# Kernel optimization log

Measured on AMD Instinct MI355X. Metric: run time of the kernel, lower is better.

The kernel has to match this reference:

```python
import jax, jax.numpy as jnp
import numpy as np

B, N, D, E, R, K = 4, 2048, 1024, 8, 256, 2


def setup_inputs() -> dict:
    key = jax.random.key(0)
    ks = jax.random.split(key, 5)
    scale = 0.02
    return {
        "x": jax.random.normal(ks[0], (B, N, D), dtype=jnp.float32),
        "gate_w": jax.random.normal(ks[1], (D, E), dtype=jnp.float32) * scale,
        "Wu": jax.random.normal(ks[2], (E, D, R), dtype=jnp.float32) * scale,
        "Wv": jax.random.normal(ks[3], (E, D, R), dtype=jnp.float32) * scale,
        "Wo": jax.random.normal(ks[4], (E, R, D), dtype=jnp.float32) * scale,
    }


def reference(x, gate_w, Wu, Wv, Wo):
    # Router: top-k over expert logits, softmax over the selected k logits.
    logits = jnp.einsum("bnd,de->bne", x, gate_w)          # [B,N,E]
    topv, topi = jax.lax.top_k(logits, K)                    # [B,N,K]
    w = jax.nn.softmax(topv, axis=-1)                        # [B,N,K]

    # Dense all-expert SwiGLU (matches reference semantics: every expert
    # computed for every token, then gathered by top-k index).
    u = jnp.einsum("bnd,edr->bner", x, Wu)                  # [B,N,E,R]
    v = jnp.einsum("bnd,edr->bner", x, Wv)                  # [B,N,E,R]
    s = jax.nn.silu(u) * v                                   # [B,N,E,R]
    Y = jnp.einsum("bner,erd->bned", s, Wo)                 # [B,N,E,D]

    # Gather the k selected experts per token and combine with gate weights.
    y_sel = jnp.take_along_axis(Y, topi[..., None], axis=2)  # [B,N,K,D]
    out = jnp.einsum("bnkd,bnk->bnd", y_sel, w)             # [B,N,D]
    return out
```

## Files before the change

### kernel.cpp

```cpp
#include <hip/hip_runtime.h>
#include <math.h>

#define BN 8192
#define DIM 1024
#define NE 8
#define RR 256

using bf16x8 = __attribute__((ext_vector_type(8))) short;
using f32x4  = __attribute__((ext_vector_type(4))) float;

__device__ inline unsigned short f2bf(float f) {
    unsigned int u = __float_as_uint(f);
    u = (u + 0x7fffu + ((u >> 16) & 1u)) >> 16;
    return (unsigned short)u;
}

__global__ __launch_bounds__(256) void k_gwt(const float* __restrict__ gw,
                                             float* __restrict__ gwT) {
    int i = blockIdx.x * 256 + threadIdx.x;
    float v = gw[i];
    int d = i >> 3, e = i & 7;
    gwT[e * DIM + d] = v;
}

__global__ __launch_bounds__(256) void k_router3(const float* __restrict__ x,
                                                 const float* __restrict__ gwT,
                                                 int* __restrict__ topi,
                                                 float* __restrict__ topw,
                                                 unsigned short* __restrict__ xb) {
    int wid  = (blockIdx.x * blockDim.x + threadIdx.x) >> 6;
    int lane = threadIdx.x & 63;
    const float* xp = x + (size_t)wid * DIM + lane * 4;
    unsigned short* xbp = xb + (size_t)wid * DIM + lane * 4;
    float4 acc[NE];
#pragma unroll
    for (int e = 0; e < NE; ++e) acc[e] = float4{0.f, 0.f, 0.f, 0.f};
#pragma unroll
    for (int k = 0; k < 4; ++k) {
        float4 xv = *(const float4*)(xp + k * 256);
        ushort4 us = { f2bf(xv.x), f2bf(xv.y), f2bf(xv.z), f2bf(xv.w) };
        *(ushort4*)(xbp + k * 256) = us;
#pragma unroll
        for (int e = 0; e < NE; ++e) {
            float4 gv = *(const float4*)(gwT + e * DIM + k * 256 + lane * 4);
            acc[e].x += xv.x * gv.x; acc[e].y += xv.y * gv.y;
            acc[e].z += xv.z * gv.z; acc[e].w += xv.w * gv.w;
        }
    }
    float lg[NE];
#pragma unroll
    for (int e = 0; e < NE; ++e)
        lg[e] = (acc[e].x + acc[e].y) + (acc[e].z + acc[e].w);
#pragma unroll
    for (int off = 32; off; off >>= 1) {
#pragma unroll
        for (int e = 0; e < NE; ++e) lg[e] += __shfl_xor(lg[e], off, 64);
    }
    if (lane == 0) {
        float best = lg[0]; int bi = 0;
#pragma unroll
        for (int e = 1; e < NE; ++e) if (lg[e] > best) { best = lg[e]; bi = e; }
        float sec = -3.4e38f; int si = 0;
#pragma unroll
        for (int e = 0; e < NE; ++e) if (e != bi && lg[e] > sec) { sec = lg[e]; si = e; }
        float p  = __expf(sec - best);
        float w0 = 1.f / (1.f + p);
        float w1 = p * w0;
        topi[wid * 2 + 0] = bi;  topw[wid * 2 + 0] = w0;
        topi[wid * 2 + 1] = si;  topw[wid * 2 + 1] = w1;
    }
}

__global__ __launch_bounds__(1024) void k_count_scan(const int* __restrict__ topi,
                                                     int* __restrict__ counts,
                                                     int* __restrict__ offsets,
                                                     int* __restrict__ fill,
                                                     int* __restrict__ tileOff) {
    __shared__ int sh[1024 * NE];
    int tid = threadIdx.x;
    int c[NE];
#pragma unroll
    for (int j = 0; j < NE; ++j) c[j] = 0;
    const int4* tp = (const int4*)topi;
    for (int i = tid; i < BN * 2 / 4; i += 1024) {
        int4 v = tp[i];
#pragma unroll
        for (int j = 0; j < NE; ++j)
            c[j] += (v.x == j) + (v.y == j) + (v.z == j) + (v.w == j);
    }
#pragma unroll
    for (int j = 0; j < NE; ++j) sh[tid * NE + j] = c[j];
    __syncthreads();
    for (int s = 512; s > 0; s >>= 1) {
        if (tid < s) {
#pragma unroll
            for (int j = 0; j < NE; ++j) sh[tid * NE + j] += sh[(tid + s) * NE + j];
        }
        __syncthreads();
    }
    if (tid == 0) {
        int acc = 0, tacc = 0;
        for (int j = 0; j < NE; ++j) {
            int cj = sh[j];
            counts[j]  = cj;
            offsets[j] = acc;   acc  += cj;
            tileOff[j] = tacc;  tacc += (cj + 63) >> 6;
        }
        tileOff[NE] = tacc;
    }
    if (tid < NE) fill[tid] = 0;
}

__global__ __launch_bounds__(256) void k_fill2(const int* __restrict__ topi,
                                               const float* __restrict__ topw,
                                               const int* __restrict__ offsets,
                                               int* __restrict__ fill,
                                               int* __restrict__ btok,
                                               float* __restrict__ bw,
                                               int* __restrict__ slotOf) {
    int tid = threadIdx.x;
    int i = blockIdx.x * 256 + tid;
    int w = tid >> 6, lane = tid & 63;
    int e = topi[i];
    float wt = topw[i];

    __shared__ int waveCnt[4][NE];
    __shared__ int wavePre[4][NE];
    __shared__ int baseSh[NE];

    int myrank = 0;
    unsigned long long lt = (1ull << lane) - 1ull;
#pragma unroll
    for (int j = 0; j < NE; ++j) {
        unsigned long long m = __ballot(e == j);
        if (e == j) myrank = __popcll(m & lt);
        if (lane == 0) waveCnt[w][j] = __popcll(m);
    }
    __syncthreads();
    if (tid < NE) {
        int j = tid, acc = 0;
#pragma unroll
        for (int ww = 0; ww < 4; ++ww) { wavePre[ww][j] = acc; acc += waveCnt[ww][j]; }
        baseSh[j] = atomicAdd(&fill[j], acc);
    }
    __syncthreads();
    int slot = offsets[e] + baseSh[e] + wavePre[w][e] + myrank;
    btok[slot] = i >> 1;
    bw[slot]   = wt;
    slotOf[i]  = slot;
}

__global__ __launch_bounds__(256) void k_cvt3(const float* __restrict__ Wu,
                                              const float* __restrict__ Wv,
                                              const float* __restrict__ Wo,
                                              unsigned short* __restrict__ Wub,
                                              unsigned short* __restrict__ Wvb,
                                              unsigned short* __restrict__ Wob) {
    int z = blockIdx.y;
    int which = z >> 3, e = z & 7;
    int tile = blockIdx.x;
    const float* in; unsigned short* out;
    int M, N, n0, m0;
    if (which < 2) {
        M = DIM; N = RR;
        n0 = (tile & 7) * 32;  m0 = (tile >> 3) * 32;
        in = which ? Wv : Wu;  out = which ? Wvb : Wub;
    } else {
        M = RR; N = DIM;
        n0 = (tile & 31) * 32; m0 = (tile >> 5) * 32;
        in = Wo; out = Wob;
    }
    __shared__ float t[32][33];
    int tx = threadIdx.x & 31, ty = threadIdx.x >> 5;
    const float* inE = in + (size_t)e * M * N;
    unsigned short* outE = out + (size_t)e * M * N;
#pragma unroll
    for (int i = ty; i < 32; i += 8)
        t[i][tx] = inE[(size_t)(m0 + i) * N + n0 + tx];
    __syncthreads();
#pragma unroll
    for (int i = ty; i < 32; i += 8)
        outE[(size_t)(n0 + i) * M + m0 + tx] = f2bf(t[tx][i]);
}

__global__ __launch_bounds__(256, 2) void k_uv(
        const unsigned short* __restrict__ xb,
        const unsigned short* __restrict__ Wub,
        const unsigned short* __restrict__ Wvb,
        const int* __restrict__ counts,
        const int* __restrict__ offsets,
        const int* __restrict__ tileOff,
        const int* __restrict__ btok,
        const float* __restrict__ bw,
        unsigned short* __restrict__ Sbuf) {
    int bid = blockIdx.x;
    int lt  = (bid & 7) * 66 + (bid >> 3);
    int rh  = lt & 1;
    int mt_lin = lt >> 1;
    if (mt_lin >= tileOff[NE]) return;
    int e = 0;
#pragma unroll
    for (int j = 1; j < NE; ++j) if (mt_lin >= tileOff[j]) e = j;
    int t0 = (mt_lin - tileOff[e]) * 64;
    int ne = counts[e];
    int nt = min(64, ne - t0);
    int start = offsets[e] + t0;

    int tid = threadIdx.x;
    int w = tid >> 6, lane = tid & 63;
    int m16 = lane & 15, quad = lane >> 4;

    __shared__ unsigned short As[2][64][72];
    __shared__ int   tokL[64];
    __shared__ float gwL[64];

    if (tid < 64) {
        tokL[tid] = (tid < nt) ? btok[start + tid] : btok[start];
        gwL[tid]  = (tid < nt) ? bw[start + tid] : 0.f;
    }
    __syncthreads();

    const unsigned short* WuE = Wub + (size_t)e * RR * DIM;
    const unsigned short* WvE = Wvb + (size_t)e * RR * DIM;

    int arow = tid >> 2, apart = tid & 3;
    const unsigned short* asrc = xb + (size_t)tokL[arow] * DIM + apart * 16;

    const unsigned short* buBase = WuE + (size_t)(rh * 128 + w * 32 + m16) * DIM + quad * 8;
    const unsigned short* bvBase = WvE + (size_t)(rh * 128 + w * 32 + m16) * DIM + quad * 8;

    f32x4 accU[4][2], accV[4][2];
    f32x4 zz = {0.f, 0.f, 0.f, 0.f};
#pragma unroll
    for (int mt = 0; mt < 4; ++mt)
#pragma unroll
        for (int nl = 0; nl < 2; ++nl) { accU[mt][nl] = zz; accV[mt][nl] = zz; }

    uint4 pa0 = *(const uint4*)(asrc);
    uint4 pa1 = *(const uint4*)(asrc + 8);
    uint4 bu[2][2][2], bv[2][2][2];
#pragma unroll
    for (int ks = 0; ks < 2; ++ks)
#pragma unroll
        for (int nl = 0; nl < 2; ++nl) {
            bu[0][ks][nl] = *(const uint4*)(buBase + (size_t)nl * 16 * DIM + ks * 32);
            bv[0][ks][nl] = *(const uint4*)(bvBase + (size_t)nl * 16 * DIM + ks * 32);
        }

#pragma unroll
    for (int kt = 0; kt < 16; ++kt) {
        const int cur = kt & 1, nxt = cur ^ 1;
        *(uint4*)&As[cur][arow][apart * 16]     = pa0;
        *(uint4*)&As[cur][arow][apart * 16 + 8] = pa1;
        if (kt < 15) {
            pa0 = *(const uint4*)(asrc + (kt + 1) * 64);
            pa1 = *(const uint4*)(asrc + (kt + 1) * 64 + 8);
#pragma unroll
            for (int ks = 0; ks < 2; ++ks)
#pragma unroll
                for (int nl = 0; nl < 2; ++nl) {
                    bu[nxt][ks][nl] = *(const uint4*)(buBase + (size_t)nl * 16 * DIM + (kt + 1) * 64 + ks * 32);
                    bv[nxt][ks][nl] = *(const uint4*)(bvBase + (size_t)nl * 16 * DIM + (kt + 1) * 64 + ks * 32);
                }
        }
        __syncthreads();
#pragma unroll
        for (int ks = 0; ks < 2; ++ks) {
            bf16x8 a[4];
#pragma unroll
            for (int mt = 0; mt < 4; ++mt)
                a[mt] = *(const bf16x8*)&As[cur][mt * 16 + m16][ks * 32 + quad * 8];
#pragma unroll
            for (int nl = 0; nl < 2; ++nl) {
                bf16x8 fu = __builtin_bit_cast(bf16x8, bu[cur][ks][nl]);
                bf16x8 fv = __builtin_bit_cast(bf16x8, bv[cur][ks][nl]);
#pragma unroll
                for (int mt = 0; mt < 4; ++mt) {
                    accU[mt][nl] = __builtin_amdgcn_mfma_f32_16x16x32_bf16(a[mt], fu, accU[mt][nl], 0, 0, 0);
                    accV[mt][nl] = __builtin_amdgcn_mfma_f32_16x16x32_bf16(a[mt], fv, accV[mt][nl], 0, 0, 0);
                }
            }
        }
    }

#pragma unroll
    for (int mt = 0; mt < 4; ++mt)
#pragma unroll
        for (int nl = 0; nl < 2; ++nl)
#pragma unroll
            for (int reg = 0; reg < 4; ++reg) {
                int trow = mt * 16 + quad * 4 + reg;
                int rcol = rh * 128 + w * 32 + nl * 16 + m16;
                float u = accU[mt][nl][reg], v = accV[mt][nl][reg];
                float s = (u / (1.f + __expf(-u))) * v * gwL[trow];
                if (trow < nt)
                    Sbuf[(size_t)(start + trow) * RR + rcol] = f2bf(s);
            }
}

__global__ __launch_bounds__(256, 2) void k_down(
        const unsigned short* __restrict__ Sbuf,
        const unsigned short* __restrict__ Wob,
        const int* __restrict__ counts,
        const int* __restrict__ offsets,
        const int* __restrict__ tileOff,
        const int* __restrict__ btok,
        float* __restrict__ ybuf,
        float* __restrict__ out) {
    int bid = blockIdx.x;
    int lt  = (bid & 7) * 132 + (bid >> 3);
    int nd = lt & 3;
    int mt_lin = lt >> 2;
    if (mt_lin >= tileOff[NE]) return;
    int e = 0;
#pragma unroll
    for (int j = 1; j < NE; ++j) if (mt_lin >= tileOff[j]) e = j;
    int t0 = (mt_lin - tileOff[e]) * 64;
    int ne = counts[e];
    int nt = min(64, ne - t0);
    int start = offsets[e] + t0;

    int tid = threadIdx.x;
    int w = tid >> 6, lane = tid & 63;
    int m16 = lane & 15, quad = lane >> 4;

    __shared__ unsigned short As[2][64][72];
    __shared__ int tokL[64];

    if (tid < 64)
        tokL[tid] = (tid < nt) ? btok[start + tid] : btok[start];
    __syncthreads();

    const unsigned short* WoE = Wob + (size_t)e * DIM * RR;

    int arow = tid >> 2, apart = tid & 3;
    const unsigned short* asrc = Sbuf + (size_t)(start + arow) * RR + apart * 16;

    const unsigned short* bBase = WoE + (size_t)(nd * 256 + w * 64 + m16) * RR + quad * 8;

    f32x4 acc[4][4];
    f32x4 zz = {0.f, 0.f, 0.f, 0.f};
#pragma unroll
    for (int mt = 0; mt < 4; ++mt)
#pragma unroll
        for (int nl = 0; nl < 4; ++nl) acc[mt][nl] = zz;

    uint4 pa0 = *(const uint4*)(asrc);
    uint4 pa1 = *(const uint4*)(asrc + 8);
    uint4 b[2][2][4];
#pragma unroll
    for (int ks = 0; ks < 2; ++ks)
#pragma unroll
        for (int nl = 0; nl < 4; ++nl)
            b[0][ks][nl] = *(const uint4*)(bBase + (size_t)nl * 16 * RR + ks * 32);

#pragma unroll
    for (int kt = 0; kt < 4; ++kt) {
        const int cur = kt & 1, nxt = cur ^ 1;
        *(uint4*)&As[cur][arow][apart * 16]     = pa0;
        *(uint4*)&As[cur][arow][apart * 16 + 8] = pa1;
        if (kt < 3) {
            pa0 = *(const uint4*)(asrc + (kt + 1) * 64);
            pa1 = *(const uint4*)(asrc + (kt + 1) * 64 + 8);
#pragma unroll
            for (int ks = 0; ks < 2; ++ks)
#pragma unroll
                for (int nl = 0; nl < 4; ++nl)
                    b[nxt][ks][nl] = *(const uint4*)(bBase + (size_t)nl * 16 * RR + (kt + 1) * 64 + ks * 32);
        }
        __syncthreads();
#pragma unroll
        for (int ks = 0; ks < 2; ++ks) {
            bf16x8 a[4];
#pragma unroll
            for (int mt = 0; mt < 4; ++mt)
                a[mt] = *(const bf16x8*)&As[cur][mt * 16 + m16][ks * 32 + quad * 8];
#pragma unroll
            for (int nl = 0; nl < 4; ++nl) {
                bf16x8 fb = __builtin_bit_cast(bf16x8, b[cur][ks][nl]);
#pragma unroll
                for (int mt = 0; mt < 4; ++mt)
                    acc[mt][nl] = __builtin_amdgcn_mfma_f32_16x16x32_bf16(a[mt], fb, acc[mt][nl], 0, 0, 0);
            }
        }
    }

    if (ybuf) {
#pragma unroll
        for (int mt = 0; mt < 4; ++mt)
#pragma unroll
            for (int nl = 0; nl < 4; ++nl)
#pragma unroll
                for (int reg = 0; reg < 4; ++reg) {
                    int srow = mt * 16 + quad * 4 + reg;
                    int d    = nd * 256 + w * 64 + nl * 16 + m16;
                    if (srow < nt)
                        ybuf[(size_t)(start + srow) * DIM + d] = acc[mt][nl][reg];
                }
    } else {
#pragma unroll
        for (int mt = 0; mt < 4; ++mt)
#pragma unroll
            for (int nl = 0; nl < 4; ++nl)
#pragma unroll
                for (int reg = 0; reg < 4; ++reg) {
                    int srow = mt * 16 + quad * 4 + reg;
                    int d    = nd * 256 + w * 64 + nl * 16 + m16;
                    if (srow < nt)
                        atomicAdd(&out[(size_t)tokL[srow] * DIM + d], acc[mt][nl][reg]);
                }
    }
}

__global__ __launch_bounds__(256) void k_combine(const float* __restrict__ ybuf,
                                                 const int* __restrict__ slotOf,
                                                 float* __restrict__ out) {
    int t   = blockIdx.x;
    int seg = threadIdx.x;
    int s0 = slotOf[t * 2 + 0];
    int s1 = slotOf[t * 2 + 1];
    float4 a = *(const float4*)(ybuf + (size_t)s0 * DIM + seg * 4);
    float4 b = *(const float4*)(ybuf + (size_t)s1 * DIM + seg * 4);
    float4 r = { a.x + b.x, a.y + b.y, a.z + b.z, a.w + b.w };
    *(float4*)(out + (size_t)t * DIM + seg * 4) = r;
}

extern "C" void kernel_launch(void* const* d_in, const int* in_sizes, int n_in,
                              void* d_out, int out_size, void* d_ws, size_t ws_size,
                              hipStream_t stream) {
    const float* x  = (const float*)d_in[0];
    const float* gw = (const float*)d_in[1];
    const float* Wu = (const float*)d_in[2];
    const float* Wv = (const float*)d_in[3];
    const float* Wo = (const float*)d_in[4];
    float* out = (float*)d_out;

    int*   wsi     = (int*)d_ws;
    int*   counts  = wsi + 0;
    int*   offsets = wsi + 8;
    int*   fill    = wsi + 16;
    int*   tileOff = wsi + 24;
    int*   topi    = wsi + 48;
    float* topw    = (float*)(wsi + 48 + 16384);
    int*   btok    = wsi + 48 + 32768;
    float* bw      = (float*)(wsi + 48 + 49152);
    int*   slotOf  = wsi + 48 + 65536;
    float* gwT     = (float*)((char*)d_ws + 327872);

    const size_t off_xb  = 393216;
    const size_t off_wub = off_xb  + (size_t)BN * DIM * 2;
    const size_t off_wvb = off_wub + (size_t)NE * RR * DIM * 2;
    const size_t off_wob = off_wvb + (size_t)NE * RR * DIM * 2;
    const size_t off_sb  = off_wob + (size_t)NE * DIM * RR * 2;
    const size_t off_yb  = off_sb  + (size_t)(BN * 2 + 128) * RR * 2;
    const size_t need_yb = off_yb  + (size_t)BN * 2 * DIM * 4;

    unsigned short* xb   = (unsigned short*)((char*)d_ws + off_xb);
    unsigned short* Wub  = (unsigned short*)((char*)d_ws + off_wub);
    unsigned short* Wvb  = (unsigned short*)((char*)d_ws + off_wvb);
    unsigned short* Wob  = (unsigned short*)((char*)d_ws + off_wob);
    unsigned short* Sbuf = (unsigned short*)((char*)d_ws + off_sb);
    bool use_ybuf = (ws_size >= need_yb);
    float* ybuf = use_ybuf ? (float*)((char*)d_ws + off_yb) : nullptr;

    k_gwt<<<dim3(DIM * NE / 256), 256, 0, stream>>>(gw, gwT);
    k_router3<<<dim3(BN / 4), 256, 0, stream>>>(x, gwT, topi, topw, xb);
    k_count_scan<<<1, 1024, 0, stream>>>(topi, counts, offsets, fill, tileOff);
    k_fill2<<<dim3(BN * 2 / 256), 256, 0, stream>>>(topi, topw, offsets, fill,
                                                    btok, bw, slotOf);
    k_cvt3<<<dim3(256, 24), 256, 0, stream>>>(Wu, Wv, Wo, Wub, Wvb, Wob);

    if (!use_ybuf)
        hipMemsetAsync(d_out, 0, (size_t)BN * DIM * sizeof(float), stream);

    k_uv<<<dim3(528), 256, 0, stream>>>(xb, Wub, Wvb, counts, offsets, tileOff,
                                        btok, bw, Sbuf);
    k_down<<<dim3(1056), 256, 0, stream>>>(Sbuf, Wob, counts, offsets, tileOff,
                                           btok, ybuf, out);
    if (use_ybuf)
        k_combine<<<dim3(BN), 256, 0, stream>>>(ybuf, slotOf, out);
}
```

Before: 225.5 us.

## Use 128-token tiles with direct global-to-LDS loads and swizzled shared layout

The grouped-expert GEMMs now use 128-token M tiles (tile offsets recomputed in the scan) with a 2x2 wave layout. Both A and B operands are staged into LDS via global_load_lds with an XOR swizzle instead of register-staged double buffering. Larger tiles are meant to raise weight reuse per block and cut global traffic, while direct-to-LDS loads save VGPRs and instructions. In exchange, loads are no longer overlapped with compute (single buffer, two barriers per k-step), and the larger tile wastes more rows on padded, partially filled expert tiles.

```diff
diff --git a/kernel.cpp b/kernel.cpp
--- a/kernel.cpp
+++ b/kernel.cpp
@@ -8,6 +8,10 @@
 
 using bf16x8 = __attribute__((ext_vector_type(8))) short;
 using f32x4  = __attribute__((ext_vector_type(4))) float;
+
+#define GLD16(g, l) __builtin_amdgcn_global_load_lds(                      \
+    (const __attribute__((address_space(1))) void*)(g),                    \
+    (__attribute__((address_space(3))) void*)(l), 16, 0, 0)
 
 __device__ inline unsigned short f2bf(float f) {
     unsigned int u = __float_as_uint(f);
@@ -104,7 +108,7 @@
             int cj = sh[j];
             counts[j]  = cj;
             offsets[j] = acc;   acc  += cj;
-            tileOff[j] = tacc;  tacc += (cj + 63) >> 6;
+            tileOff[j] = tacc;  tacc += (cj + 127) >> 7;
         }
         tileOff[NE] = tacc;
     }
@@ -194,40 +198,55 @@
         const float* __restrict__ bw,
         unsigned short* __restrict__ Sbuf) {
     int bid = blockIdx.x;
-    int lt  = (bid & 7) * 66 + (bid >> 3);
-    int rh  = lt & 1;
-    int mt_lin = lt >> 1;
+    int lt  = (bid & 7) * 68 + (bid >> 3);
+    int rt  = lt & 3;
+    int mt_lin = lt >> 2;
     if (mt_lin >= tileOff[NE]) return;
     int e = 0;
 #pragma unroll
     for (int j = 1; j < NE; ++j) if (mt_lin >= tileOff[j]) e = j;
-    int t0 = (mt_lin - tileOff[e]) * 64;
+    int t0 = (mt_lin - tileOff[e]) * 128;
     int ne = counts[e];
-    int nt = min(64, ne - t0);
+    int nt = min(128, ne - t0);
     int start = offsets[e] + t0;
 
     int tid = threadIdx.x;
     int w = tid >> 6, lane = tid & 63;
     int m16 = lane & 15, quad = lane >> 4;
-
-    __shared__ unsigned short As[2][64][72];
-    __shared__ int   tokL[64];
-    __shared__ float gwL[64];
-
-    if (tid < 64) {
+    int wm = w & 1, wn = w >> 1;
+
+    __shared__ unsigned short As[128][64];
+    __shared__ unsigned short Bs[128][64];
+    __shared__ int   tokL[128];
+    __shared__ float gwL[128];
+
+    if (tid < 128) {
         tokL[tid] = (tid < nt) ? btok[start + tid] : btok[start];
         gwL[tid]  = (tid < nt) ? bw[start + tid] : 0.f;
     }
     __syncthreads();
 
+    int rc0 = rt * 64;
     const unsigned short* WuE = Wub + (size_t)e * RR * DIM;
     const unsigned short* WvE = Wvb + (size_t)e * RR * DIM;
 
-    int arow = tid >> 2, apart = tid & 3;
-    const unsigned short* asrc = xb + (size_t)tokL[arow] * DIM + apart * 16;
-
-    const unsigned short* buBase = WuE + (size_t)(rh * 128 + w * 32 + m16) * DIM + quad * 8;
-    const unsigned short* bvBase = WvE + (size_t)(rh * 128 + w * 32 + m16) * DIM + quad * 8;
+    const unsigned short* aS[4];
+    const unsigned short* bS[4];
+    int dstOff[4];
+#pragma unroll
+    for (int i = 0; i < 4; ++i) {
+        int chunk = w * 4 + i;
+        int row = chunk * 8 + (lane >> 3);
+        int js  = (lane & 7) ^ (row & 7);
+        aS[i] = xb + (size_t)tokL[row] * DIM + js * 8;
+        bS[i] = ((row < 64) ? (WuE + (size_t)(rc0 + row) * DIM)
+                            : (WvE + (size_t)(rc0 + row - 64) * DIM)) + js * 8;
+        dstOff[i] = chunk * 1024;
+    }
+    auto* asb = (__attribute__((address_space(3))) char*)&As[0][0];
+    auto* bsb = (__attribute__((address_space(3))) char*)&Bs[0][0];
+    const char* Ab = (const char*)&As[0][0];
+    const char* Bb = (const char*)&Bs[0][0];
 
     f32x4 accU[4][2], accV[4][2];
     f32x4 zz = {0.f, 0.f, 0.f, 0.f};
@@ -236,51 +255,38 @@
 #pragma unroll
         for (int nl = 0; nl < 2; ++nl) { accU[mt][nl] = zz; accV[mt][nl] = zz; }
 
-    uint4 pa0 = *(const uint4*)(asrc);
-    uint4 pa1 = *(const uint4*)(asrc + 8);
-    uint4 bu[2][2][2], bv[2][2][2];
-#pragma unroll
-    for (int ks = 0; ks < 2; ++ks)
-#pragma unroll
-        for (int nl = 0; nl < 2; ++nl) {
-            bu[0][ks][nl] = *(const uint4*)(buBase + (size_t)nl * 16 * DIM + ks * 32);
-            bv[0][ks][nl] = *(const uint4*)(bvBase + (size_t)nl * 16 * DIM + ks * 32);
-        }
-
-#pragma unroll
     for (int kt = 0; kt < 16; ++kt) {
-        const int cur = kt & 1, nxt = cur ^ 1;
-        *(uint4*)&As[cur][arow][apart * 16]     = pa0;
-        *(uint4*)&As[cur][arow][apart * 16 + 8] = pa1;
-        if (kt < 15) {
-            pa0 = *(const uint4*)(asrc + (kt + 1) * 64);
-            pa1 = *(const uint4*)(asrc + (kt + 1) * 64 + 8);
-#pragma unroll
-            for (int ks = 0; ks < 2; ++ks)
-#pragma unroll
-                for (int nl = 0; nl < 2; ++nl) {
-                    bu[nxt][ks][nl] = *(const uint4*)(buBase + (size_t)nl * 16 * DIM + (kt + 1) * 64 + ks * 32);
-                    bv[nxt][ks][nl] = *(const uint4*)(bvBase + (size_t)nl * 16 * DIM + (kt + 1) * 64 + ks * 32);
+        if (kt) __syncthreads();
+#pragma unroll
+        for (int i = 0; i < 4; ++i) {
+            GLD16(aS[i] + kt * 64, asb + dstOff[i]);
+            GLD16(bS[i] + kt * 64, bsb + dstOff[i]);
+        }
+        __syncthreads();
+#pragma unroll
+        for (int ks = 0; ks < 2; ++ks) {
+            bf16x8 a[4], bu[2], bv[2];
+#pragma unroll
+            for (int mt = 0; mt < 4; ++mt) {
+                int r = wm * 64 + mt * 16 + m16;
+                int u = (ks * 4 + quad) ^ (r & 7);
+                a[mt] = *(const bf16x8*)(Ab + r * 128 + u * 16);
+            }
+#pragma unroll
+            for (int nl = 0; nl < 2; ++nl) {
+                int r = wn * 32 + nl * 16 + m16;
+                int u = (ks * 4 + quad) ^ (r & 7);
+                bu[nl] = *(const bf16x8*)(Bb + r * 128 + u * 16);
+                bv[nl] = *(const bf16x8*)(Bb + (r + 64) * 128 + u * 16);
+            }
+#pragma unroll
+            for (int nl = 0; nl < 2; ++nl)
+#pragma unroll
+                for (int mt = 0; mt < 4; ++mt) {
+                    accU[mt][nl] = __builtin_amdgcn_mfma_f32_16x16x32_bf16(a[mt], bu[nl], accU[mt][nl], 0, 0, 0);
+                    accV[mt][nl] = __builtin_amdgcn_mfma_f32_16x16x32_bf16(a[mt], bv[nl], accV[mt][nl], 0, 0, 0);
                 }
         }
-        __syncthreads();
-#pragma unroll
-        for (int ks = 0; ks < 2; ++ks) {
-            bf16x8 a[4];
-#pragma unroll
-            for (int mt = 0; mt < 4; ++mt)
-                a[mt] = *(const bf16x8*)&As[cur][mt * 16 + m16][ks * 32 + quad * 8];
-#pragma unroll
-            for (int nl = 0; nl < 2; ++nl) {
-                bf16x8 fu = __builtin_bit_cast(bf16x8, bu[cur][ks][nl]);
-                bf16x8 fv = __builtin_bit_cast(bf16x8, bv[cur][ks][nl]);
-#pragma unroll
-                for (int mt = 0; mt < 4; ++mt) {
-                    accU[mt][nl] = __builtin_amdgcn_mfma_f32_16x16x32_bf16(a[mt], fu, accU[mt][nl], 0, 0, 0);
-                    accV[mt][nl] = __builtin_amdgcn_mfma_f32_16x16x32_bf16(a[mt], fv, accV[mt][nl], 0, 0, 0);
-                }
-            }
-        }
     }
 
 #pragma unroll
@@ -289,8 +295,8 @@
         for (int nl = 0; nl < 2; ++nl)
 #pragma unroll
             for (int reg = 0; reg < 4; ++reg) {
-                int trow = mt * 16 + quad * 4 + reg;
-                int rcol = rh * 128 + w * 32 + nl * 16 + m16;
+                int trow = wm * 64 + mt * 16 + quad * 4 + reg;
+                int rcol = rc0 + wn * 32 + nl * 16 + m16;
                 float u = accU[mt][nl][reg], v = accV[mt][nl][reg];
                 float s = (u / (1.f + __expf(-u))) * v * gwL[trow];
                 if (trow < nt)
@@ -308,35 +314,49 @@
         float* __restrict__ ybuf,
         float* __restrict__ out) {
     int bid = blockIdx.x;
-    int lt  = (bid & 7) * 132 + (bid >> 3);
-    int nd = lt & 3;
-    int mt_lin = lt >> 2;
+    int lt  = (bid & 7) * 136 + (bid >> 3);
+    int nd = lt & 7;
+    int mt_lin = lt >> 3;
     if (mt_lin >= tileOff[NE]) return;
     int e = 0;
 #pragma unroll
     for (int j = 1; j < NE; ++j) if (mt_lin >= tileOff[j]) e = j;
-    int t0 = (mt_lin - tileOff[e]) * 64;
+    int t0 = (mt_lin - tileOff[e]) * 128;
     int ne = counts[e];
-    int nt = min(64, ne - t0);
+    int nt = min(128, ne - t0);
     int start = offsets[e] + t0;
 
     int tid = threadIdx.x;
     int w = tid >> 6, lane = tid & 63;
     int m16 = lane & 15, quad = lane >> 4;
-
-    __shared__ unsigned short As[2][64][72];
-    __shared__ int tokL[64];
-
-    if (tid < 64)
+    int wm = w & 1, wn = w >> 1;
+
+    __shared__ unsigned short As[128][64];
+    __shared__ unsigned short Bs[128][64];
+    __shared__ int tokL[128];
+
+    if (tid < 128)
         tokL[tid] = (tid < nt) ? btok[start + tid] : btok[start];
     __syncthreads();
 
     const unsigned short* WoE = Wob + (size_t)e * DIM * RR;
 
-    int arow = tid >> 2, apart = tid & 3;
-    const unsigned short* asrc = Sbuf + (size_t)(start + arow) * RR + apart * 16;
-
-    const unsigned short* bBase = WoE + (size_t)(nd * 256 + w * 64 + m16) * RR + quad * 8;
+    const unsigned short* aS[4];
+    const unsigned short* bS[4];
+    int dstOff[4];
+#pragma unroll
+    for (int i = 0; i < 4; ++i) {
+        int chunk = w * 4 + i;
+        int row = chunk * 8 + (lane >> 3);
+        int js  = (lane & 7) ^ (row & 7);
+        aS[i] = Sbuf + (size_t)(start + row) * RR + js * 8;
+        bS[i] = WoE + (size_t)(nd * 128 + row) * RR + js * 8;
+        dstOff[i] = chunk * 1024;
+    }
+    auto* asb = (__attribute__((address_space(3))) char*)&As[0][0];
+    auto* bsb = (__attribute__((address_space(3))) char*)&Bs[0][0];
+    const char* Ab = (const char*)&As[0][0];
+    const char* Bb = (const char*)&Bs[0][0];
 
     f32x4 acc[4][4];
     f32x4 zz = {0.f, 0.f, 0.f, 0.f};
@@ -345,43 +365,34 @@
 #pragma unroll
         for (int nl = 0; nl < 4; ++nl) acc[mt][nl] = zz;
 
-    uint4 pa0 = *(const uint4*)(asrc);
-    uint4 pa1 = *(const uint4*)(asrc + 8);
-    uint4 b[2][2][4];
-#pragma unroll
-    for (int ks = 0; ks < 2; ++ks)
-#pragma unroll
-        for (int nl = 0; nl < 4; ++nl)
-            b[0][ks][nl] = *(const uint4*)(bBase + (size_t)nl * 16 * RR + ks * 32);
-
-#pragma unroll
     for (int kt = 0; kt < 4; ++kt) {
-        const int cur = kt & 1, nxt = cur ^ 1;
-        *(uint4*)&As[cur][arow][apart * 16]     = pa0;
-        *(uint4*)&As[cur][arow][apart * 16 + 8] = pa1;
-        if (kt < 3) {
-            pa0 = *(const uint4*)(asrc + (kt + 1) * 64);
-            pa1 = *(const uint4*)(asrc + (kt + 1) * 64 + 8);
-#pragma unroll
-            for (int ks = 0; ks < 2; ++ks)
-#pragma unroll
-                for (int nl = 0; nl < 4; ++nl)
-                    b[nxt][ks][nl] = *(const uint4*)(bBase + (size_t)nl * 16 * RR + (kt + 1) * 64 + ks * 32);
+        if (kt) __syncthreads();
+#pragma unroll
+        for (int i = 0; i < 4; ++i) {
+            GLD16(aS[i] + kt * 64, asb + dstOff[i]);
+            GLD16(bS[i] + kt * 64, bsb + dstOff[i]);
         }
         __syncthreads();
 #pragma unroll
         for (int ks = 0; ks < 2; ++ks) {
-            bf16x8 a[4];
-#pragma unroll
-            for (int mt = 0; mt < 4; ++mt)
-                a[mt] = *(const bf16x8*)&As[cur][mt * 16 + m16][ks * 32 + quad * 8];
+            bf16x8 a[4], b[4];
+#pragma unroll
+            for (int mt = 0; mt < 4; ++mt) {
+                int r = wm * 64 + mt * 16 + m16;
+                int u = (ks * 4 + quad) ^ (r & 7);
+                a[mt] = *(const bf16x8*)(Ab + r * 128 + u * 16);
+            }
 #pragma unroll
             for (int nl = 0; nl < 4; ++nl) {
-                bf16x8 fb = __builtin_bit_cast(bf16x8, b[cur][ks][nl]);
+                int r = wn * 64 + nl * 16 + m16;
+                int u = (ks * 4 + quad) ^ (r & 7);
+                b[nl] = *(const bf16x8*)(Bb + r * 128 + u * 16);
+            }
+#pragma unroll
+            for (int nl = 0; nl < 4; ++nl)
 #pragma unroll
                 for (int mt = 0; mt < 4; ++mt)
-                    acc[mt][nl] = __builtin_amdgcn_mfma_f32_16x16x32_bf16(a[mt], fb, acc[mt][nl], 0, 0, 0);
-            }
+                    acc[mt][nl] = __builtin_amdgcn_mfma_f32_16x16x32_bf16(a[mt], b[nl], acc[mt][nl], 0, 0, 0);
         }
     }
 
@@ -392,8 +403,8 @@
             for (int nl = 0; nl < 4; ++nl)
 #pragma unroll
                 for (int reg = 0; reg < 4; ++reg) {
-                    int srow = mt * 16 + quad * 4 + reg;
-                    int d    = nd * 256 + w * 64 + nl * 16 + m16;
+                    int srow = wm * 64 + mt * 16 + quad * 4 + reg;
+                    int d    = nd * 128 + wn * 64 + nl * 16 + m16;
                     if (srow < nt)
                         ybuf[(size_t)(start + srow) * DIM + d] = acc[mt][nl][reg];
                 }
@@ -404,8 +415,8 @@
             for (int nl = 0; nl < 4; ++nl)
 #pragma unroll
                 for (int reg = 0; reg < 4; ++reg) {
-                    int srow = mt * 16 + quad * 4 + reg;
-                    int d    = nd * 256 + w * 64 + nl * 16 + m16;
+                    int srow = wm * 64 + mt * 16 + quad * 4 + reg;
+                    int d    = nd * 128 + wn * 64 + nl * 16 + m16;
                     if (srow < nt)
                         atomicAdd(&out[(size_t)tokL[srow] * DIM + d], acc[mt][nl][reg]);
                 }
@@ -473,9 +484,9 @@
     if (!use_ybuf)
         hipMemsetAsync(d_out, 0, (size_t)BN * DIM * sizeof(float), stream);
 
-    k_uv<<<dim3(528), 256, 0, stream>>>(xb, Wub, Wvb, counts, offsets, tileOff,
+    k_uv<<<dim3(544), 256, 0, stream>>>(xb, Wub, Wvb, counts, offsets, tileOff,
                                         btok, bw, Sbuf);
-    k_down<<<dim3(1056), 256, 0, stream>>>(Sbuf, Wob, counts, offsets, tileOff,
+    k_down<<<dim3(1088), 256, 0, stream>>>(Sbuf, Wob, counts, offsets, tileOff,
                                            btok, ybuf, out);
     if (use_ybuf)
         k_combine<<<dim3(BN), 256, 0, stream>>>(ybuf, slotOf, out);
```

After: 195.7 us. -13.2%, faster.
